# Performance work log

Hardware: AMD Instinct MI355X
Metric: run time of the kernel (lower is better)

The kernel has to match this reference:

```python
import math
import jax, jax.numpy as jnp
import numpy as np

LMAX = 2


def _cg_complex(j1, m1, j2, m2, j3, m3):
    # Standard (Racah) Clebsch-Gordan coefficient <j1 m1 j2 m2 | j3 m3> for integer l.
    if m1 + m2 != m3 or j3 < abs(j1 - j2) or j3 > j1 + j2:
        return 0.0
    f = math.factorial
    pre = math.sqrt((2 * j3 + 1) * f(j3 + j1 - j2) * f(j3 - j1 + j2) * f(j1 + j2 - j3) / f(j1 + j2 + j3 + 1))
    pre *= math.sqrt(f(j3 + m3) * f(j3 - m3) * f(j1 - m1) * f(j1 + m1) * f(j2 - m2) * f(j2 + m2))
    kmin = max(0, j2 - j3 - m1, j1 + m2 - j3)
    kmax = min(j1 + j2 - j3, j1 - m1, j2 + m2)
    s = 0.0
    for k in range(kmin, kmax + 1):
        s += (-1.0) ** k / (f(k) * f(j1 + j2 - j3 - k) * f(j1 - m1 - k) * f(j2 + m2 - k) * f(j3 - j2 + m1 + k) * f(j3 - j1 - m2 + k))
    return pre * s


def _u_matrix(l):
    # Unitary map from complex SH (Condon-Shortley) to real SH, rows = real mu, cols = complex m.
    U = np.zeros((2 * l + 1, 2 * l + 1), dtype=np.complex128)
    U[l, l] = 1.0
    isq2 = 1.0 / math.sqrt(2.0)
    for m in range(1, l + 1):
        U[l + m, l - m] = isq2
        U[l + m, l + m] = ((-1.0) ** m) * isq2
        U[l - m, l - m] = 1j * isq2
        U[l - m, l + m] = -1j * ((-1.0) ** m) * isq2
    return U


def _real_clebsch_gordan(lmax):
    # Dense real-SH CG tensor over combined s=(l,m) indices, shape [S,S,S], S=(lmax+1)^2.
    S = (lmax + 1) ** 2
    cg = np.zeros((S, S, S))
    for l1 in range(lmax + 1):
        for l2 in range(lmax + 1):
            for l3 in range(abs(l1 - l2), min(lmax, l1 + l2) + 1):
                blk = np.zeros((2 * l1 + 1, 2 * l2 + 1, 2 * l3 + 1))
                for i1, m1 in enumerate(range(-l1, l1 + 1)):
                    for i2, m2 in enumerate(range(-l2, l2 + 1)):
                        for i3, m3 in enumerate(range(-l3, l3 + 1)):
                            blk[i1, i2, i3] = _cg_complex(l1, m1, l2, m2, l3, m3)
                U1, U2, U3 = _u_matrix(l1), _u_matrix(l2), _u_matrix(l3)
                r = np.einsum('am,bn,co,mno->abc', U1, U2, U3.conj(), blk.astype(np.complex128))
                r = r.real if (l1 + l2 + l3) % 2 == 0 else r.imag  # parity-dependent real part
                cg[l1 * l1:(l1 + 1) ** 2, l2 * l2:(l2 + 1) ** 2, l3 * l3:(l3 + 1) ** 2] = r
    return cg


def _sparse_cg(lmax):
    cg = _real_clebsch_gordan(lmax)
    i1, i2, i3 = np.nonzero(np.abs(cg) > 1e-10)
    vals = cg[i1, i2, i3].astype(np.float32)
    widx = np.floor(np.sqrt(i3.astype(np.float64))).astype(np.int32)  # l of output combined index
    return vals, i1.astype(np.int32), i2.astype(np.int32), i3.astype(np.int32), widx


def _spherical_harmonics_l2(d):
    # Real SH up to l=2, 'component' normalization (|x|=1 assumed). Order: (l,m) = (0,0),(1,-1),(1,0),(1,1),(2,-2..2).
    x, y, z = d[..., 0], d[..., 1], d[..., 2]
    s3, s5, s15 = math.sqrt(3.0), math.sqrt(5.0), math.sqrt(15.0)
    return jnp.stack([
        jnp.ones_like(x),
        s3 * y, s3 * z, s3 * x,
        s15 * x * y, s15 * y * z, 0.5 * s5 * (3.0 * z * z - 1.0), s15 * x * z, 0.5 * s15 * (x * x - y * y),
    ], axis=-1)


def setup_inputs():
    N_ATOMS, N_EDGES, N_BASIS, N_RADIAL = 1200, 12000, 128, 20
    S = (LMAX + 1) ** 2
    key = jax.random.key(0)
    ks = jax.random.split(key, 8)
    vals, i1, i2, i3, widx = _sparse_cg(LMAX)
    return {
        'x': jax.random.normal(ks[0], (N_ATOMS, S, N_BASIS), jnp.float32),
        'radial_ij': jax.random.uniform(ks[1], (N_EDGES, N_RADIAL), jnp.float32),
        'dir_ij': jax.random.normal(ks[2], (N_EDGES, 3), jnp.float32),
        'cutoff_ij': jax.random.uniform(ks[3], (N_EDGES, 1), jnp.float32),
        'W_filter': jax.random.normal(ks[6], (N_RADIAL, N_BASIS * (LMAX + 1)), jnp.float32) / math.sqrt(N_RADIAL),
        'b_filter': jnp.zeros((N_BASIS * (LMAX + 1),), jnp.float32),
        'cg_vals': jnp.asarray(vals),
        'idx_i': jax.random.randint(ks[4], (N_EDGES,), 0, N_ATOMS),
        'idx_j': jax.random.randint(ks[5], (N_EDGES,), 0, N_ATOMS),
        'cg_idx_in1': jnp.asarray(i1),
        'cg_idx_in2': jnp.asarray(i2),
        'cg_idx_out': jnp.asarray(i3),
        'w_idx': jnp.asarray(widx),
    }


def reference(x, radial_ij, dir_ij, cutoff_ij, W_filter, b_filter, cg_vals,
              idx_i, idx_j, cg_idx_in1, cg_idx_in2, cg_idx_out, w_idx):
    n_atoms, S, F = x.shape
    E = dir_ij.shape[0]
    d = dir_ij / jnp.linalg.norm(dir_ij, axis=-1, keepdims=True)
    Y = _spherical_harmonics_l2(d)                        # [E, S]
    Wij = (radial_ij @ W_filter + b_filter) * cutoff_ij   # [E, (lmax+1)*F]
    Wij = Wij.reshape(E, LMAX + 1, F)                     # per-l radial filter
    xj = x[idx_j]                                         # [E, S, F] neighbor features
    # Sparse CG tensor-product contraction over combined (l,m) indices.
    v = (Y[:, cg_idx_in2, None] * cg_vals[None, :, None]
         * Wij[:, w_idx, :] * xj[:, cg_idx_in1, :])       # [E, n_cg, F]
    yij = jnp.zeros((E, S, F), v.dtype).at[:, cg_idx_out, :].add(v)
    return jax.ops.segment_sum(yij, idx_i, num_segments=n_atoms)
```

## Files before the change

kernel.cpp:

```cpp
#include <hip/hip_runtime.h>
#include <math.h>


#define S9     9
#define MROW   12
#define NF     128
#define NRAD   20
#define TEDGE  8
#define MAXA   2048
#define EMAX   12288

__global__ __launch_bounds__(1024) void csr_kernel(
    const int* __restrict__ idx_i, int E, int A,
    int* __restrict__ offsets,
    int* __restrict__ esorted)
{
    __shared__ int lcnt[MAXA];
    __shared__ int wtot[16];
    __shared__ int esh[EMAX];
    const int t = threadIdx.x;
    const int lane = t & 63;
    const int wid  = t >> 6;

    for (int i = t; i < A; i += 1024) lcnt[i] = 0;
    __syncthreads();
    for (int e = t; e < E; e += 1024) atomicAdd(&lcnt[idx_i[e]], 1);
    __syncthreads();

    const int i0 = 2 * t, i1 = 2 * t + 1;
    const int ca = (i0 < A) ? lcnt[i0] : 0;
    const int cb = (i1 < A) ? lcnt[i1] : 0;
    __syncthreads();

    int inc = ca + cb;
    #pragma unroll
    for (int d = 1; d < 64; d <<= 1) {
        int u = __shfl_up(inc, d);
        if (lane >= d) inc += u;
    }
    if (lane == 63) wtot[wid] = inc;
    __syncthreads();
    if (wid == 0) {
        int w = (lane < 16) ? wtot[lane] : 0;
        #pragma unroll
        for (int d = 1; d < 16; d <<= 1) {
            int u = __shfl_up(w, d);
            if (lane >= d) w += u;
        }
        if (lane < 16) wtot[lane] = w;
    }
    __syncthreads();
    int run = ((wid > 0) ? wtot[wid - 1] : 0) + (inc - (ca + cb));
    if (i0 < A) { offsets[i0] = run; lcnt[i0] = run; run += ca; }
    if (i1 < A) { offsets[i1] = run; lcnt[i1] = run; run += cb; }
    if (t == 1023) offsets[A] = wtot[15];
    __syncthreads();

    if (E <= EMAX) {
        for (int e = t; e < E; e += 1024) {
            int p = atomicAdd(&lcnt[idx_i[e]], 1);
            esh[p] = e;
        }
        __syncthreads();
        for (int i = t; i < E; i += 1024) esorted[i] = esh[i];
    } else {
        for (int e = t; e < E; e += 1024) {
            int p = atomicAdd(&lcnt[idx_i[e]], 1);
            esorted[p] = e;
        }
    }
}

__global__ __launch_bounds__(64) void so3_atom_kernel(
    const float* __restrict__ x,
    const float* __restrict__ radial,
    const float* __restrict__ dir,
    const float* __restrict__ cutoff,
    const float* __restrict__ Wf,
    const float* __restrict__ bf,
    const float* __restrict__ cg_vals,
    const int* __restrict__ idx_j,
    const int* __restrict__ cg_i1,
    const int* __restrict__ cg_i2,
    const int* __restrict__ cg_i3,
    int ncg,
    const int* __restrict__ offsets,
    const int* __restrict__ esorted,
    float* __restrict__ out)
{
    const int a  = blockIdx.x >> 1;
    const int fh = blockIdx.x & 1;
    const int t  = threadIdx.x;
    const int f  = fh * 64 + t;
    const int e0 = offsets[a];
    const int e1 = offsets[a + 1];

    __shared__ __align__(16) float M[TEDGE][MROW * S9];
    __shared__ float Ysh[TEDGE][S9];
    __shared__ float radsh[TEDGE][NRAD];
    __shared__ float cutsh[TEDGE];
    __shared__ int   jsh[TEDGE];

    float acc[S9];
    #pragma unroll
    for (int s = 0; s < S9; ++s) acc[s] = 0.f;

    const float b0 = bf[0 * NF + f];
    const float b1 = bf[1 * NF + f];
    const float b2 = bf[2 * NF + f];

    for (int base = e0; base < e1; base += TEDGE) {
        const int n = min(TEDGE, e1 - base);

        {
            float4* Mz = (float4*)&M[0][0];
            const int tot4 = TEDGE * MROW * S9 / 4;
            for (int qq = t; qq < tot4; qq += 64) Mz[qq] = make_float4(0.f, 0.f, 0.f, 0.f);
        }
        if (t < TEDGE) {
            int jj = a;
            float cut = 0.f;
            if (t < n) {
                const int e = esorted[base + t];
                jj = idx_j[e];
                cut = cutoff[e];
                float dx = dir[3 * e], dy = dir[3 * e + 1], dz = dir[3 * e + 2];
                const float inv = rsqrtf(dx * dx + dy * dy + dz * dz);
                dx *= inv; dy *= inv; dz *= inv;
                const float s3c  = 1.7320508075688772f;
                const float s5c  = 2.2360679774997896f;
                const float s15c = 3.8729833462074170f;
                Ysh[t][0] = 1.0f;
                Ysh[t][1] = s3c * dy;
                Ysh[t][2] = s3c * dz;
                Ysh[t][3] = s3c * dx;
                Ysh[t][4] = s15c * dx * dy;
                Ysh[t][5] = s15c * dy * dz;
                Ysh[t][6] = 0.5f * s5c * (3.0f * dz * dz - 1.0f);
                Ysh[t][7] = s15c * dx * dz;
                Ysh[t][8] = 0.5f * s15c * (dx * dx - dy * dy);
            }
            jsh[t] = jj;
            cutsh[t] = cut;
        }
        for (int qq = t; qq < TEDGE * NRAD; qq += 64) {
            const int c = qq / NRAD;
            const int r = qq - c * NRAD;
            radsh[c][r] = (c < n) ? radial[(size_t)esorted[base + c] * NRAD + r] : 0.f;
        }
        __syncthreads();

        float w[TEDGE][3];
        #pragma unroll
        for (int c = 0; c < TEDGE; ++c) { w[c][0] = b0; w[c][1] = b1; w[c][2] = b2; }
        #pragma unroll 4
        for (int r = 0; r < NRAD; ++r) {
            const float* wrow = Wf + r * (3 * NF) + f;
            const float w0 = wrow[0];
            const float w1 = wrow[NF];
            const float w2 = wrow[2 * NF];
            #pragma unroll
            for (int c = 0; c < TEDGE; ++c) {
                const float rv = radsh[c][r];
                w[c][0] = fmaf(rv, w0, w[c][0]);
                w[c][1] = fmaf(rv, w1, w[c][1]);
                w[c][2] = fmaf(rv, w2, w[c][2]);
            }
        }
        #pragma unroll
        for (int c = 0; c < TEDGE; ++c) {
            const float cut = cutsh[c];
            w[c][0] *= cut; w[c][1] *= cut; w[c][2] *= cut;
        }

        {
            const int c = t >> 3;
            const int r = t & 7;
            if (c < n) {
                for (int kk = r; kk < ncg; kk += 8) {
                    atomicAdd(&M[c][cg_i3[kk] * MROW + cg_i1[kk]],
                              cg_vals[kk] * Ysh[c][cg_i2[kk]]);
                }
            }
        }
        __syncthreads();

        #pragma unroll
        for (int g = 0; g < 2; ++g) {
            float xj[4][S9];
            #pragma unroll
            for (int c2 = 0; c2 < 4; ++c2) {
                const int j = __builtin_amdgcn_readfirstlane(jsh[g * 4 + c2]);
                const float* xp = x + (size_t)j * (S9 * NF) + f;
                #pragma unroll
                for (int s = 0; s < S9; ++s) xj[c2][s] = xp[s * NF];
            }
            #pragma unroll
            for (int c2 = 0; c2 < 4; ++c2) {
                const int c = g * 4 + c2;
                #pragma unroll
                for (int s3 = 0; s3 < S9; ++s3) {
                    const float4* mr = (const float4*)&M[c][s3 * MROW];
                    const float4 m0 = mr[0];
                    const float4 m1 = mr[1];
                    const float  m8 = M[c][s3 * MROW + 8];
                    float ts = m0.x * xj[c2][0];
                    ts = fmaf(m0.y, xj[c2][1], ts);
                    ts = fmaf(m0.z, xj[c2][2], ts);
                    ts = fmaf(m0.w, xj[c2][3], ts);
                    ts = fmaf(m1.x, xj[c2][4], ts);
                    ts = fmaf(m1.y, xj[c2][5], ts);
                    ts = fmaf(m1.z, xj[c2][6], ts);
                    ts = fmaf(m1.w, xj[c2][7], ts);
                    ts = fmaf(m8,   xj[c2][8], ts);
                    const float wl = (s3 == 0) ? w[c][0] : ((s3 < 4) ? w[c][1] : w[c][2]);
                    acc[s3] = fmaf(wl, ts, acc[s3]);
                }
            }
        }
        __syncthreads();
    }

    float* op = out + (size_t)a * (S9 * NF) + f;
    #pragma unroll
    for (int s = 0; s < S9; ++s) op[s * NF] = acc[s];
}

extern "C" void kernel_launch(void* const* d_in, const int* in_sizes, int n_in,
                              void* d_out, int out_size, void* d_ws, size_t ws_size,
                              hipStream_t stream) {
    const float* x       = (const float*)d_in[0];
    const float* radial  = (const float*)d_in[1];
    const float* dir     = (const float*)d_in[2];
    const float* cutoff  = (const float*)d_in[3];
    const float* Wf      = (const float*)d_in[4];
    const float* bf      = (const float*)d_in[5];
    const float* cg_vals = (const float*)d_in[6];
    const int*   idx_i   = (const int*)d_in[7];
    const int*   idx_j   = (const int*)d_in[8];
    const int*   cg_i1   = (const int*)d_in[9];
    const int*   cg_i2   = (const int*)d_in[10];
    const int*   cg_i3   = (const int*)d_in[11];

    const int E   = in_sizes[7];
    const int ncg = in_sizes[6];
    const int A   = in_sizes[0] / (S9 * NF);

    int* offsets = (int*)d_ws;
    int* esorted = offsets + (A + 1);

    csr_kernel<<<1, 1024, 0, stream>>>(idx_i, E, A, offsets, esorted);

    so3_atom_kernel<<<2 * A, 64, 0, stream>>>(
        x, radial, dir, cutoff, Wf, bf, cg_vals, idx_j,
        cg_i1, cg_i2, cg_i3, ncg, offsets, esorted, (float*)d_out);
}
```

Before: 146.6 us.

## Split per-edge CG matrix and radial filter into separate edge-parallel kernel

Moves computation of the per-edge CG-contracted Y matrix and the radial filter weights out of the per-atom kernel into a new edge-parallel kernel that writes them to workspace. The atom gather kernel then only loads these precomputed values plus neighbor features, uses 128 threads per atom instead of two 64-thread blocks, and stages edge indices in windows. This removes the duplicated per-feature-half work and the serialized shared-memory atomics from the gather critical path, at the cost of an extra launch and extra global traffic for the workspace buffers (E*108 + E*384 floats).

```diff
diff --git a/kernel.cpp b/kernel.cpp
--- a/kernel.cpp
+++ b/kernel.cpp
@@ -4,9 +4,11 @@
 
 #define S9     9
 #define MROW   12
+#define MSZ    (S9 * MROW)
 #define NF     128
 #define NRAD   20
 #define TEDGE  8
+#define WIN    96
 #define MAXA   2048
 #define EMAX   12288
 
@@ -71,154 +73,180 @@
     }
 }
 
-__global__ __launch_bounds__(64) void so3_atom_kernel(
-    const float* __restrict__ x,
+__global__ __launch_bounds__(256) void so3_edge_kernel(
     const float* __restrict__ radial,
     const float* __restrict__ dir,
     const float* __restrict__ cutoff,
     const float* __restrict__ Wf,
     const float* __restrict__ bf,
     const float* __restrict__ cg_vals,
-    const int* __restrict__ idx_j,
     const int* __restrict__ cg_i1,
     const int* __restrict__ cg_i2,
     const int* __restrict__ cg_i3,
-    int ncg,
+    int ncg, int E,
+    float* __restrict__ Mws,
+    float* __restrict__ Wws)
+{
+    const int wid  = threadIdx.x >> 6;
+    const int lane = threadIdx.x & 63;
+    const int e = blockIdx.x * 4 + wid;
+    if (e >= E) return;
+
+    __shared__ __align__(16) float Msh[4][MSZ];
+    __shared__ float Ysh[4][S9];
+
+    if (lane < 27) ((float4*)&Msh[wid][0])[lane] = make_float4(0.f, 0.f, 0.f, 0.f);
+
+    float dx = dir[3 * e], dy = dir[3 * e + 1], dz = dir[3 * e + 2];
+    const float inv = rsqrtf(dx * dx + dy * dy + dz * dz);
+    dx *= inv; dy *= inv; dz *= inv;
+    const float s3c  = 1.7320508075688772f;
+    const float s5c  = 2.2360679774997896f;
+    const float s15c = 3.8729833462074170f;
+    if (lane == 0) {
+        Ysh[wid][0] = 1.0f;
+        Ysh[wid][1] = s3c * dy;
+        Ysh[wid][2] = s3c * dz;
+        Ysh[wid][3] = s3c * dx;
+        Ysh[wid][4] = s15c * dx * dy;
+        Ysh[wid][5] = s15c * dy * dz;
+        Ysh[wid][6] = 0.5f * s5c * (3.0f * dz * dz - 1.0f);
+        Ysh[wid][7] = s15c * dx * dz;
+        Ysh[wid][8] = 0.5f * s15c * (dx * dx - dy * dy);
+    }
+
+    float rad[NRAD];
+    #pragma unroll
+    for (int r = 0; r < NRAD; ++r) rad[r] = radial[(size_t)e * NRAD + r];
+    const float cut = cutoff[e];
+
+    for (int k = lane; k < ncg; k += 64) {
+        atomicAdd(&Msh[wid][cg_i3[k] * MROW + cg_i1[k]],
+                  cg_vals[k] * Ysh[wid][cg_i2[k]]);
+    }
+
+    const int f0 = lane, f1 = lane + 64;
+    float a00 = bf[0 * NF + f0], a01 = bf[0 * NF + f1];
+    float a10 = bf[1 * NF + f0], a11 = bf[1 * NF + f1];
+    float a20 = bf[2 * NF + f0], a21 = bf[2 * NF + f1];
+    #pragma unroll 4
+    for (int r = 0; r < NRAD; ++r) {
+        const float* wr = Wf + r * (3 * NF);
+        a00 = fmaf(rad[r], wr[0 * NF + f0], a00);
+        a01 = fmaf(rad[r], wr[0 * NF + f1], a01);
+        a10 = fmaf(rad[r], wr[1 * NF + f0], a10);
+        a11 = fmaf(rad[r], wr[1 * NF + f1], a11);
+        a20 = fmaf(rad[r], wr[2 * NF + f0], a20);
+        a21 = fmaf(rad[r], wr[2 * NF + f1], a21);
+    }
+    float* wout = Wws + (size_t)e * (3 * NF);
+    wout[0 * NF + f0] = a00 * cut; wout[0 * NF + f1] = a01 * cut;
+    wout[1 * NF + f0] = a10 * cut; wout[1 * NF + f1] = a11 * cut;
+    wout[2 * NF + f0] = a20 * cut; wout[2 * NF + f1] = a21 * cut;
+
+    if (lane < 27) {
+        float4 v = ((const float4*)&Msh[wid][0])[lane];
+        ((float4*)(Mws + (size_t)e * MSZ))[lane] = v;
+    }
+}
+
+__global__ __launch_bounds__(128) void so3_gather_kernel(
+    const float* __restrict__ x,
+    const float* __restrict__ Mws,
+    const float* __restrict__ Wws,
+    const int* __restrict__ idx_j,
     const int* __restrict__ offsets,
     const int* __restrict__ esorted,
     float* __restrict__ out)
 {
-    const int a  = blockIdx.x >> 1;
-    const int fh = blockIdx.x & 1;
-    const int t  = threadIdx.x;
-    const int f  = fh * 64 + t;
+    const int a    = blockIdx.x;
+    const int t    = threadIdx.x;
+    const int lane = t & 63;
+    const int fh   = t >> 6;
+    const int f    = fh * 64 + lane;
     const int e0 = offsets[a];
     const int e1 = offsets[a + 1];
 
-    __shared__ __align__(16) float M[TEDGE][MROW * S9];
-    __shared__ float Ysh[TEDGE][S9];
-    __shared__ float radsh[TEDGE][NRAD];
-    __shared__ float cutsh[TEDGE];
-    __shared__ int   jsh[TEDGE];
+    __shared__ __align__(16) float M2[TEDGE * MSZ];
+    __shared__ int eall[WIN], jall[WIN];
 
     float acc[S9];
     #pragma unroll
     for (int s = 0; s < S9; ++s) acc[s] = 0.f;
 
-    const float b0 = bf[0 * NF + f];
-    const float b1 = bf[1 * NF + f];
-    const float b2 = bf[2 * NF + f];
-
-    for (int base = e0; base < e1; base += TEDGE) {
-        const int n = min(TEDGE, e1 - base);
-
-        {
-            float4* Mz = (float4*)&M[0][0];
-            const int tot4 = TEDGE * MROW * S9 / 4;
-            for (int qq = t; qq < tot4; qq += 64) Mz[qq] = make_float4(0.f, 0.f, 0.f, 0.f);
-        }
-        if (t < TEDGE) {
-            int jj = a;
-            float cut = 0.f;
-            if (t < n) {
-                const int e = esorted[base + t];
-                jj = idx_j[e];
-                cut = cutoff[e];
-                float dx = dir[3 * e], dy = dir[3 * e + 1], dz = dir[3 * e + 2];
-                const float inv = rsqrtf(dx * dx + dy * dy + dz * dz);
-                dx *= inv; dy *= inv; dz *= inv;
-                const float s3c  = 1.7320508075688772f;
-                const float s5c  = 2.2360679774997896f;
-                const float s15c = 3.8729833462074170f;
-                Ysh[t][0] = 1.0f;
-                Ysh[t][1] = s3c * dy;
-                Ysh[t][2] = s3c * dz;
-                Ysh[t][3] = s3c * dx;
-                Ysh[t][4] = s15c * dx * dy;
-                Ysh[t][5] = s15c * dy * dz;
-                Ysh[t][6] = 0.5f * s5c * (3.0f * dz * dz - 1.0f);
-                Ysh[t][7] = s15c * dx * dz;
-                Ysh[t][8] = 0.5f * s15c * (dx * dx - dy * dy);
+    for (int w0 = e0; w0 < e1; w0 += WIN) {
+        const int wn = min(WIN, e1 - w0);
+        __syncthreads();
+        for (int i = t; i < wn; i += 128) {
+            const int e = esorted[w0 + i];
+            eall[i] = e;
+            jall[i] = idx_j[e];
+        }
+        __syncthreads();
+
+        for (int base = 0; base < wn; base += TEDGE) {
+            const int n = min(TEDGE, wn - base);
+
+            for (int qq = t; qq < TEDGE * 27; qq += 128) {
+                const int c = qq / 27;
+                float4 v = make_float4(0.f, 0.f, 0.f, 0.f);
+                if (c < n)
+                    v = ((const float4*)(Mws + (size_t)eall[base + c] * MSZ))[qq - c * 27];
+                ((float4*)M2)[qq] = v;
             }
-            jsh[t] = jj;
-            cutsh[t] = cut;
-        }
-        for (int qq = t; qq < TEDGE * NRAD; qq += 64) {
-            const int c = qq / NRAD;
-            const int r = qq - c * NRAD;
-            radsh[c][r] = (c < n) ? radial[(size_t)esorted[base + c] * NRAD + r] : 0.f;
-        }
-        __syncthreads();
-
-        float w[TEDGE][3];
-        #pragma unroll
-        for (int c = 0; c < TEDGE; ++c) { w[c][0] = b0; w[c][1] = b1; w[c][2] = b2; }
-        #pragma unroll 4
-        for (int r = 0; r < NRAD; ++r) {
-            const float* wrow = Wf + r * (3 * NF) + f;
-            const float w0 = wrow[0];
-            const float w1 = wrow[NF];
-            const float w2 = wrow[2 * NF];
+
+            float wreg[TEDGE][3];
+            int jreg[TEDGE];
             #pragma unroll
             for (int c = 0; c < TEDGE; ++c) {
-                const float rv = radsh[c][r];
-                w[c][0] = fmaf(rv, w0, w[c][0]);
-                w[c][1] = fmaf(rv, w1, w[c][1]);
-                w[c][2] = fmaf(rv, w2, w[c][2]);
-            }
-        }
-        #pragma unroll
-        for (int c = 0; c < TEDGE; ++c) {
-            const float cut = cutsh[c];
-            w[c][0] *= cut; w[c][1] *= cut; w[c][2] *= cut;
-        }
-
-        {
-            const int c = t >> 3;
-            const int r = t & 7;
-            if (c < n) {
-                for (int kk = r; kk < ncg; kk += 8) {
-                    atomicAdd(&M[c][cg_i3[kk] * MROW + cg_i1[kk]],
-                              cg_vals[kk] * Ysh[c][cg_i2[kk]]);
+                if (c < n) {
+                    const float* wp = Wws + (size_t)eall[base + c] * (3 * NF) + f;
+                    wreg[c][0] = wp[0];
+                    wreg[c][1] = wp[NF];
+                    wreg[c][2] = wp[2 * NF];
+                    jreg[c] = __builtin_amdgcn_readfirstlane(jall[base + c]);
+                } else {
+                    wreg[c][0] = wreg[c][1] = wreg[c][2] = 0.f;
+                    jreg[c] = a;
                 }
             }
-        }
-        __syncthreads();
-
-        #pragma unroll
-        for (int g = 0; g < 2; ++g) {
-            float xj[4][S9];
+            __syncthreads();
+
             #pragma unroll
-            for (int c2 = 0; c2 < 4; ++c2) {
-                const int j = __builtin_amdgcn_readfirstlane(jsh[g * 4 + c2]);
-                const float* xp = x + (size_t)j * (S9 * NF) + f;
+            for (int g = 0; g < 2; ++g) {
+                float xj[4][S9];
                 #pragma unroll
-                for (int s = 0; s < S9; ++s) xj[c2][s] = xp[s * NF];
-            }
-            #pragma unroll
-            for (int c2 = 0; c2 < 4; ++c2) {
-                const int c = g * 4 + c2;
+                for (int c2 = 0; c2 < 4; ++c2) {
+                    const float* xp = x + (size_t)jreg[g * 4 + c2] * (S9 * NF) + f;
+                    #pragma unroll
+                    for (int s = 0; s < S9; ++s) xj[c2][s] = xp[s * NF];
+                }
                 #pragma unroll
-                for (int s3 = 0; s3 < S9; ++s3) {
-                    const float4* mr = (const float4*)&M[c][s3 * MROW];
-                    const float4 m0 = mr[0];
-                    const float4 m1 = mr[1];
-                    const float  m8 = M[c][s3 * MROW + 8];
-                    float ts = m0.x * xj[c2][0];
-                    ts = fmaf(m0.y, xj[c2][1], ts);
-                    ts = fmaf(m0.z, xj[c2][2], ts);
-                    ts = fmaf(m0.w, xj[c2][3], ts);
-                    ts = fmaf(m1.x, xj[c2][4], ts);
-                    ts = fmaf(m1.y, xj[c2][5], ts);
-                    ts = fmaf(m1.z, xj[c2][6], ts);
-                    ts = fmaf(m1.w, xj[c2][7], ts);
-                    ts = fmaf(m8,   xj[c2][8], ts);
-                    const float wl = (s3 == 0) ? w[c][0] : ((s3 < 4) ? w[c][1] : w[c][2]);
-                    acc[s3] = fmaf(wl, ts, acc[s3]);
+                for (int c2 = 0; c2 < 4; ++c2) {
+                    const int c = g * 4 + c2;
+                    #pragma unroll
+                    for (int s3 = 0; s3 < S9; ++s3) {
+                        const float4* mr = (const float4*)&M2[c * MSZ + s3 * MROW];
+                        const float4 m0 = mr[0];
+                        const float4 m1 = mr[1];
+                        const float  m8 = M2[c * MSZ + s3 * MROW + 8];
+                        float ts = m0.x * xj[c2][0];
+                        ts = fmaf(m0.y, xj[c2][1], ts);
+                        ts = fmaf(m0.z, xj[c2][2], ts);
+                        ts = fmaf(m0.w, xj[c2][3], ts);
+                        ts = fmaf(m1.x, xj[c2][4], ts);
+                        ts = fmaf(m1.y, xj[c2][5], ts);
+                        ts = fmaf(m1.z, xj[c2][6], ts);
+                        ts = fmaf(m1.w, xj[c2][7], ts);
+                        ts = fmaf(m8,   xj[c2][8], ts);
+                        const float wl = (s3 == 0) ? wreg[c][0]
+                                       : ((s3 < 4) ? wreg[c][1] : wreg[c][2]);
+                        acc[s3] = fmaf(wl, ts, acc[s3]);
+                    }
                 }
             }
-        }
-        __syncthreads();
+            __syncthreads();
+        }
     }
 
     float* op = out + (size_t)a * (S9 * NF) + f;
@@ -248,10 +276,17 @@
 
     int* offsets = (int*)d_ws;
     int* esorted = offsets + (A + 1);
+    size_t ibytes = (size_t)(A + 1 + E) * sizeof(int);
+    size_t moff   = (ibytes + 255) & ~(size_t)255;
+    float* Mws = (float*)((char*)d_ws + moff);
+    float* Wws = Mws + (size_t)E * MSZ;
 
     csr_kernel<<<1, 1024, 0, stream>>>(idx_i, E, A, offsets, esorted);
 
-    so3_atom_kernel<<<2 * A, 64, 0, stream>>>(
-        x, radial, dir, cutoff, Wf, bf, cg_vals, idx_j,
-        cg_i1, cg_i2, cg_i3, ncg, offsets, esorted, (float*)d_out);
-}
+    so3_edge_kernel<<<(E + 3) / 4, 256, 0, stream>>>(
+        radial, dir, cutoff, Wf, bf, cg_vals,
+        cg_i1, cg_i2, cg_i3, ncg, E, Mws, Wws);
+
+    so3_gather_kernel<<<A, 128, 0, stream>>>(
+        x, Mws, Wws, idx_j, offsets, esorted, (float*)d_out);
+}
```

Result: faster. 135.7 us (-7.4%).
